# Kernel tuning notes

Hardware: AMD Instinct MI355X
Metric: run time of the kernel (lower is better)

The kernel has to match this reference:

```python
import jax, jax.numpy as jnp
import numpy as np
import math

D_MODEL = 1024
NHEAD = 16
D_HEAD = D_MODEL // NHEAD
TAU = 300.0
DELTA = 5.0 * 60.0  # delta_minutes -> seconds


def setup_inputs() -> dict:
    key = jax.random.key(0)
    ks = jax.random.split(key, 10)
    B, M = 4, 2048
    H = jax.random.normal(ks[0], (B, M, D_MODEL), dtype=jnp.float32)
    patch_mask = jax.random.randint(ks[1], (B, M), 0, 2).astype(jnp.int32)
    s = 1.0 / math.sqrt(D_MODEL)
    Wq = jax.random.normal(ks[2], (D_MODEL, D_MODEL), dtype=jnp.float32) * s
    bq = jnp.zeros((D_MODEL,), dtype=jnp.float32)
    Wk = jax.random.normal(ks[3], (D_MODEL, D_MODEL), dtype=jnp.float32) * s
    bk = jnp.zeros((D_MODEL,), dtype=jnp.float32)
    Wv = jax.random.normal(ks[4], (D_MODEL, D_MODEL), dtype=jnp.float32) * s
    bv = jnp.zeros((D_MODEL,), dtype=jnp.float32)
    Wo = jax.random.normal(ks[5], (D_MODEL, D_MODEL), dtype=jnp.float32) * s
    bo = jnp.zeros((D_MODEL,), dtype=jnp.float32)
    return {"H": H, "patch_mask": patch_mask, "Wq": Wq, "bq": bq,
            "Wk": Wk, "bk": bk, "Wv": Wv, "bv": bv, "Wo": Wo, "bo": bo}


def _time_bias(M):
    idx = jnp.arange(M)
    dist = jnp.abs(idx[:, None] - idx[None, :]).astype(jnp.float32) * DELTA
    w = jnp.exp(-dist / max(TAU, 1e-6))
    return jnp.log(w + 1e-12)  # (M, M)


def reference(H, patch_mask, Wq, bq, Wk, bk, Wv, bv, Wo, bo):
    B, M, D = H.shape
    nh, dh = NHEAD, D_HEAD
    # projections -> (B, nh, M, dh)
    q = (H @ Wq.T + bq).reshape(B, M, nh, dh).transpose(0, 2, 1, 3)
    k = (H @ Wk.T + bk).reshape(B, M, nh, dh).transpose(0, 2, 1, 3)
    v = (H @ Wv.T + bv).reshape(B, M, nh, dh).transpose(0, 2, 1, 3)
    attn = jnp.einsum('bhqd,bhkd->bhqk', q, k) / math.sqrt(dh)
    attn = attn + _time_bias(M)[None, None, :, :]
    key_pad = patch_mask <= 0  # (B, M)
    attn = jnp.where(key_pad[:, None, None, :], -1e9, attn)
    A = jax.nn.softmax(attn, axis=-1)
    out = jnp.einsum('bhqk,bhkd->bhqd', A, v)
    out = out.transpose(0, 2, 1, 3).reshape(B, M, D)
    out = out @ Wo.T + bo
    out = out * patch_mask[:, :, None].astype(out.dtype)
    return out
```

## Files before the change

kernel.cpp:

```cpp
#include <hip/hip_runtime.h>
#include <stdint.h>

typedef short short8 __attribute__((ext_vector_type(8)));
typedef float f32x4 __attribute__((ext_vector_type(4)));

#define B_    4
#define M_    2048
#define D_    1024
#define NH_   16
#define DH_   64
#define LOG2E 1.44269504f

__device__ __forceinline__ short f2bf(float f) {
  union { float f; uint32_t u; } v; v.f = f;
  uint32_t r = (v.u + 0x7fffu + ((v.u >> 16) & 1u)) >> 16;
  return (short)r;
}

__device__ __forceinline__ void gl_lds16(const void* g, void* l) {
  __builtin_amdgcn_global_load_lds(
      (__attribute__((address_space(1))) void*)(g),
      (__attribute__((address_space(3))) void*)(l),
      16, 0, 0);
}

__device__ __forceinline__ f32x4 mfma16(short8 a, short8 b, f32x4 c) {
  return __builtin_amdgcn_mfma_f32_16x16x32_bf16(a, b, c, 0, 0, 0);
}

__global__ __launch_bounds__(256) void cvt_all(const float* __restrict__ H,
                                               const float* __restrict__ s0,
                                               const float* __restrict__ s1,
                                               const float* __restrict__ s2,
                                               const float* __restrict__ s3,
                                               short* __restrict__ dH,
                                               short* __restrict__ d0,
                                               short* __restrict__ d1,
                                               short* __restrict__ d2,
                                               short* __restrict__ d3) {
  const int bidx = blockIdx.x;
  const float* src;
  short* dst;
  int i;
  if (bidx < 8192) {
    src = H; dst = dH; i = bidx * 256 + threadIdx.x;
  } else {
    const int y = (bidx - 8192) >> 10;
    src = (y == 0) ? s0 : (y == 1) ? s1 : (y == 2) ? s2 : s3;
    dst = (y == 0) ? d0 : (y == 1) ? d1 : (y == 2) ? d2 : d3;
    i = ((bidx - 8192) & 1023) * 256 + threadIdx.x;
  }
  float4 v = ((const float4*)src)[i];
  short4 o;
  o.x = f2bf(v.x); o.y = f2bf(v.y); o.z = f2bf(v.z); o.w = f2bf(v.w);
  ((short4*)dst)[i] = o;
}

__global__ __launch_bounds__(256, 2) void gemm_qkv(const short* __restrict__ A,
                                                   const short* __restrict__ Wqb,
                                                   const short* __restrict__ Wkb,
                                                   const short* __restrict__ Wvb,
                                                   const float* __restrict__ bq,
                                                   const float* __restrict__ bk,
                                                   const float* __restrict__ bv,
                                                   short* __restrict__ Qo,
                                                   short* __restrict__ Ko,
                                                   short* __restrict__ Vo) {
  __shared__ char smem_raw[65536];
  short* Ab0 = (short*)smem_raw;
  short* Ab1 = (short*)(smem_raw + 8192);

  const int L = blockIdx.x + 8 * blockIdx.y;
  const int xcd = L & 7;
  const int s = L >> 3;
  const int m_local = s & 7;
  const int nt = s >> 3;
  const int m0 = (xcd * 8 + m_local) * 128;
  const int n0 = nt * 128;

  const int tid = threadIdx.x;
  const int w = tid >> 6, l = tid & 63;
  const int q4 = l >> 4, c = l & 15;
  const int wr = w >> 1, wc = w & 1;

  f32x4 acc[3][4][4] = {};
  const int arow = (l >> 2);
  const int acol = ((l & 3) ^ ((l >> 3) & 3)) * 8;
  const int q4s = (q4 ^ ((c >> 1) & 3)) * 8;

  const short* Bz0 = Wqb;
  const short* Bz1 = Wkb;
  const short* Bz2 = Wvb;

#pragma unroll
  for (int st = 0; st < 2; ++st) {
    const int chunk = w * 2 + st;
    const size_t roff = (size_t)(chunk * 16 + arow) * 1024 + acol;
    gl_lds16(A + (size_t)m0 * 1024 + roff, Ab0 + chunk * 512);
    gl_lds16(Bz0 + (size_t)n0 * 1024 + roff, (short*)(smem_raw + 16384) + chunk * 512);
    gl_lds16(Bz1 + (size_t)n0 * 1024 + roff, (short*)(smem_raw + 32768) + chunk * 512);
    gl_lds16(Bz2 + (size_t)n0 * 1024 + roff, (short*)(smem_raw + 49152) + chunk * 512);
  }
  __syncthreads();

  for (int kk = 0; kk < 32; ++kk) {
    const int cur = kk & 1;
    if (kk + 1 < 32) {
      const int k0n = (kk + 1) * 32;
#pragma unroll
      for (int st = 0; st < 2; ++st) {
        const int chunk = w * 2 + st;
        const size_t roff = (size_t)(chunk * 16 + arow) * 1024 + k0n + acol;
        gl_lds16(A + (size_t)m0 * 1024 + roff, (cur ? Ab0 : Ab1) + chunk * 512);
        gl_lds16(Bz0 + (size_t)n0 * 1024 + roff,
                 (short*)(smem_raw + 16384 + (cur ? 0 : 8192)) + chunk * 512);
        gl_lds16(Bz1 + (size_t)n0 * 1024 + roff,
                 (short*)(smem_raw + 32768 + (cur ? 0 : 8192)) + chunk * 512);
        gl_lds16(Bz2 + (size_t)n0 * 1024 + roff,
                 (short*)(smem_raw + 49152 + (cur ? 0 : 8192)) + chunk * 512);
      }
    }
    const short* Ab = cur ? Ab1 : Ab0;
    short8 af[4];
#pragma unroll
    for (int i = 0; i < 4; ++i)
      af[i] = *(const short8*)(Ab + (wr * 64 + i * 16 + c) * 32 + q4s);
#pragma unroll
    for (int z = 0; z < 3; ++z) {
      const short* Bb =
          (const short*)(smem_raw + 16384 + z * 16384 + (cur ? 8192 : 0));
      short8 bfr[4];
#pragma unroll
      for (int j = 0; j < 4; ++j)
        bfr[j] = *(const short8*)(Bb + (wc * 64 + j * 16 + c) * 32 + q4s);
#pragma unroll
      for (int i = 0; i < 4; ++i)
#pragma unroll
        for (int j = 0; j < 4; ++j)
          acc[z][i][j] = mfma16(af[i], bfr[j], acc[z][i][j]);
    }
    __syncthreads();
  }

#pragma unroll
  for (int z = 0; z < 2; ++z) {
    short* Cb = (short*)smem_raw;
    const float* bias = z ? bk : bq;
    short* outp = z ? Ko : Qo;
    const float scale = z ? 1.0f : 0.125f;
#pragma unroll
    for (int j = 0; j < 4; ++j) {
      const float bvv = bias[n0 + wc * 64 + j * 16 + c];
#pragma unroll
      for (int i = 0; i < 4; ++i)
#pragma unroll
        for (int r = 0; r < 4; ++r)
          Cb[(wr * 64 + i * 16 + q4 * 4 + r) * 136 + wc * 64 + j * 16 + c] =
              f2bf((acc[z][i][j][r] + bvv) * scale);
    }
    __syncthreads();
#pragma unroll
    for (int p = 0; p < 8; ++p) {
      const int g = p * 256 + tid;
      const int row = g >> 4, seg = g & 15;
      *(short8*)(outp + (size_t)(m0 + row) * 1024 + n0 + seg * 8) =
          *(const short8*)(Cb + row * 136 + seg * 8);
    }
    __syncthreads();
  }
  {
    short* Cb = (short*)smem_raw;
#pragma unroll
    for (int j = 0; j < 4; ++j) {
      const float bvv = bv[n0 + wc * 64 + j * 16 + c];
#pragma unroll
      for (int i = 0; i < 4; ++i) {
        short4 pk;
        pk.x = f2bf(acc[2][i][j][0] + bvv);
        pk.y = f2bf(acc[2][i][j][1] + bvv);
        pk.z = f2bf(acc[2][i][j][2] + bvv);
        pk.w = f2bf(acc[2][i][j][3] + bvv);
        *(short4*)(Cb + (wc * 64 + j * 16 + c) * 136 + wr * 64 + i * 16 + q4 * 4) = pk;
      }
    }
    __syncthreads();
    const int bb = m0 >> 11;
    const int tokb = m0 & 2047;
#pragma unroll
    for (int p = 0; p < 8; ++p) {
      const int g = p * 256 + tid;
      const int col = g >> 4, rseg = g & 15;
      const int colg = n0 + col;
      const int hh = colg >> 6, dd = colg & 63;
      *(short8*)(Vo + ((size_t)(bb * NH_ + hh) * DH_ + dd) * M_ + tokb + rseg * 8) =
          *(const short8*)(Cb + col * 136 + rseg * 8);
    }
  }
}

__global__ __launch_bounds__(256, 2) void gemm_oproj(const short* __restrict__ A,
                                                     const short* __restrict__ Bt,
                                                     const float* __restrict__ bias,
                                                     const int* __restrict__ pmask,
                                                     float* __restrict__ outp) {
  __shared__ char smem[33792];
  short* Ab0 = (short*)smem;
  short* Ab1 = (short*)(smem + 8192);
  short* Bb0 = (short*)(smem + 16384);
  short* Bb1 = (short*)(smem + 24576);

  const int L = blockIdx.x + 8 * blockIdx.y;
  const int xcd = L & 7;
  const int s = L >> 3;
  const int m_local = s & 7;
  const int nt = s >> 3;
  const int m0 = (xcd * 8 + m_local) * 128;
  const int n0 = nt * 128;

  const int tid = threadIdx.x;
  const int w = tid >> 6, l = tid & 63;
  const int q4 = l >> 4, c = l & 15;
  const int wr = w >> 1, wc = w & 1;

  f32x4 acc[4][4] = {};
  const int arow = (l >> 2);
  const int acol = ((l & 3) ^ ((l >> 3) & 3)) * 8;
  const int q4s = (q4 ^ ((c >> 1) & 3)) * 8;

#pragma unroll
  for (int st = 0; st < 2; ++st) {
    const int chunk = w * 2 + st;
    const size_t roff = (size_t)(chunk * 16 + arow) * 1024 + acol;
    gl_lds16(A + (size_t)m0 * 1024 + roff, Ab0 + chunk * 512);
    gl_lds16(Bt + (size_t)n0 * 1024 + roff, Bb0 + chunk * 512);
  }
  __syncthreads();

  for (int kk = 0; kk < 32; ++kk) {
    const int cur = kk & 1;
    if (kk + 1 < 32) {
      const int k0n = (kk + 1) * 32;
#pragma unroll
      for (int st = 0; st < 2; ++st) {
        const int chunk = w * 2 + st;
        const size_t roff = (size_t)(chunk * 16 + arow) * 1024 + k0n + acol;
        gl_lds16(A + (size_t)m0 * 1024 + roff, (cur ? Ab0 : Ab1) + chunk * 512);
        gl_lds16(Bt + (size_t)n0 * 1024 + roff, (cur ? Bb0 : Bb1) + chunk * 512);
      }
    }
    const short* Ab = cur ? Ab1 : Ab0;
    const short* Bb = cur ? Bb1 : Bb0;
    short8 af[4], bfr[4];
#pragma unroll
    for (int i = 0; i < 4; ++i)
      af[i] = *(const short8*)(Ab + (wr * 64 + i * 16 + c) * 32 + q4s);
#pragma unroll
    for (int j = 0; j < 4; ++j)
      bfr[j] = *(const short8*)(Bb + (wc * 64 + j * 16 + c) * 32 + q4s);
#pragma unroll
    for (int i = 0; i < 4; ++i)
#pragma unroll
      for (int j = 0; j < 4; ++j)
        acc[i][j] = mfma16(af[i], bfr[j], acc[i][j]);
    __syncthreads();
  }

  float* Cf = (float*)smem;
#pragma unroll
  for (int half = 0; half < 2; ++half) {
    __syncthreads();
    if (wr == half) {
#pragma unroll
      for (int j = 0; j < 4; ++j) {
        const float bvv = bias[n0 + wc * 64 + j * 16 + c];
#pragma unroll
        for (int i = 0; i < 4; ++i)
#pragma unroll
          for (int r = 0; r < 4; ++r)
            Cf[(i * 16 + q4 * 4 + r) * 132 + wc * 64 + j * 16 + c] =
                acc[i][j][r] + bvv;
      }
    }
    __syncthreads();
#pragma unroll
    for (int p = 0; p < 8; ++p) {
      const int g = p * 256 + tid;
      const int row = g >> 5, seg = g & 31;
      const int rowg = m0 + half * 64 + row;
      const float mmv = (pmask[rowg] > 0) ? 1.0f : 0.0f;
      float4 v = *(const float4*)(Cf + row * 132 + seg * 4);
      v.x *= mmv; v.y *= mmv; v.z *= mmv; v.w *= mmv;
      *(float4*)(outp + (size_t)rowg * 1024 + n0 + seg * 4) = v;
    }
  }
}

__global__ __launch_bounds__(256) void attn_kernel(const short* __restrict__ Qb,
                                                   const short* __restrict__ Kb,
                                                   const short* __restrict__ Vtb,
                                                   const int* __restrict__ pmask,
                                                   short* __restrict__ Attb) {
  __shared__ char smem[20480];
  short* Ks0 = (short*)smem;
  short* Ks1 = (short*)(smem + 4096);
  short* Vs0 = (short*)(smem + 8192);
  short* Vs1 = (short*)(smem + 12288);
  short* Ps  = (short*)(smem + 16384);

  const int tid = threadIdx.x;
  const int w = tid >> 6, l = tid & 63;
  const int q4 = l >> 4, c = l & 15;
  const int qt = blockIdx.x, h = blockIdx.y, b = blockIdx.z;
  const short* Qrow = Qb + (size_t)(b * M_) * D_ + h * DH_;
  const short* Kbase = Kb + (size_t)(b * M_) * D_ + h * DH_;
  const short* Vbase = Vtb + (size_t)(b * NH_ + h) * DH_ * M_;
  const int qrow0 = qt * 64 + w * 16;

  short8 aq0 = *(const short8*)(Qrow + (size_t)(qrow0 + c) * D_ + q4 * 8);
  short8 aq1 = *(const short8*)(Qrow + (size_t)(qrow0 + c) * D_ + 32 + q4 * 8);

  const int jt0 = max(0, 2 * qt - 2);
  const int jt1 = min(M_ / 32 - 1, 2 * qt + 3);

  const int kh = tid >> 7, krow = (tid >> 2) & 31, ch = tid & 3;
  const int vrow = tid >> 2;

  {
    const int j0 = jt0 * 32;
    gl_lds16(Kbase + (size_t)(j0 + krow) * D_ + kh * 32 + ch * 8, (char*)Ks0 + tid * 16);
    gl_lds16(Vbase + (size_t)vrow * M_ + j0 + ch * 8, (char*)Vs0 + tid * 16);
  }
  __syncthreads();

  f32x4 o[4] = {};
  float lrun[4] = {0.f, 0.f, 0.f, 0.f};
  short* Pw = Ps + w * 512;

  for (int jt = jt0; jt <= jt1; ++jt) {
    const int buf = (jt - jt0) & 1;
    const int j0 = jt * 32;
    if (jt < jt1) {
      const int j0n = j0 + 32;
      gl_lds16(Kbase + (size_t)(j0n + krow) * D_ + kh * 32 + ch * 8,
               (char*)(buf ? Ks0 : Ks1) + tid * 16);
      gl_lds16(Vbase + (size_t)vrow * M_ + j0n + ch * 8,
               (char*)(buf ? Vs0 : Vs1) + tid * 16);
    }
    const short* Kt = buf ? Ks1 : Ks0;
    const short* Vt = buf ? Vs1 : Vs0;
    short8 b00 = *(const short8*)(Kt + c * 32 + q4 * 8);
    short8 b10 = *(const short8*)(Kt + 1024 + c * 32 + q4 * 8);
    short8 b01 = *(const short8*)(Kt + (16 + c) * 32 + q4 * 8);
    short8 b11 = *(const short8*)(Kt + 1024 + (16 + c) * 32 + q4 * 8);
    f32x4 s0 = {}, s1 = {};
    s0 = mfma16(aq0, b00, s0);
    s0 = mfma16(aq1, b10, s0);
    s1 = mfma16(aq0, b01, s1);
    s1 = mfma16(aq1, b11, s1);

    const float w0m = (pmask[b * M_ + j0 + c] > 0) ? 1.f : 0.f;
    const float w1m = (pmask[b * M_ + j0 + 16 + c] > 0) ? 1.f : 0.f;

#pragma unroll
    for (int r = 0; r < 4; ++r) {
      const int qr = qrow0 + q4 * 4 + r;
      const float d0 = fminf(fabsf((float)(qr - (j0 + c))), 28.0f);
      const float d1 = fminf(fabsf((float)(qr - (j0 + 16 + c))), 28.0f);
      const float p0 = exp2f((s0[r] - d0) * LOG2E) * w0m;
      const float p1 = exp2f((s1[r] - d1) * LOG2E) * w1m;
      Pw[(q4 * 4 + r) * 32 + c] = f2bf(p0);
      Pw[(q4 * 4 + r) * 32 + 16 + c] = f2bf(p1);
      lrun[r] += p0 + p1;
    }
    short8 pa = *(const short8*)(Pw + c * 32 + q4 * 8);
#pragma unroll
    for (int f = 0; f < 4; ++f) {
      short8 bv = *(const short8*)(Vt + (f * 16 + c) * 32 + q4 * 8);
      o[f] = mfma16(pa, bv, o[f]);
    }
    __syncthreads();
  }

#pragma unroll
  for (int r = 0; r < 4; ++r) {
#pragma unroll
    for (int off = 1; off < 16; off <<= 1)
      lrun[r] += __shfl_xor(lrun[r], off);
  }

  short* Cb = (short*)smem;
#pragma unroll
  for (int r = 0; r < 4; ++r) {
    const float inv = 1.0f / lrun[r];
#pragma unroll
    for (int f = 0; f < 4; ++f)
      Cb[(w * 16 + q4 * 4 + r) * 72 + f * 16 + c] = f2bf(o[f][r] * inv);
  }
  __syncthreads();
#pragma unroll
  for (int p = 0; p < 2; ++p) {
    const int u = p * 256 + tid;
    const int row = u >> 3, seg = u & 7;
    *(short8*)(Attb + (size_t)(b * M_ + qt * 64 + row) * D_ + h * DH_ + seg * 8) =
        *(const short8*)(Cb + row * 72 + seg * 8);
  }
}

extern "C" void kernel_launch(void* const* d_in, const int* in_sizes, int n_in,
                              void* d_out, int out_size, void* d_ws, size_t ws_size,
                              hipStream_t stream) {
  const float* H     = (const float*)d_in[0];
  const int*   pmask = (const int*)d_in[1];
  const float* Wq    = (const float*)d_in[2];
  const float* bq    = (const float*)d_in[3];
  const float* Wk    = (const float*)d_in[4];
  const float* bk    = (const float*)d_in[5];
  const float* Wv    = (const float*)d_in[6];
  const float* bv    = (const float*)d_in[7];
  const float* Wo    = (const float*)d_in[8];
  const float* bo    = (const float*)d_in[9];
  float* out = (float*)d_out;
  char* ws = (char*)d_ws;

  short* Hb   = (short*)(ws);
  short* Attb = (short*)(ws);
  short* Wqb  = (short*)(ws + (16u << 20));
  short* Wkb  = (short*)(ws + (18u << 20));
  short* Wvb  = (short*)(ws + (20u << 20));
  short* Wob  = (short*)(ws + (22u << 20));
  short* Qb   = (short*)(ws + (24u << 20));
  short* Kb2  = (short*)(ws + (40u << 20));
  short* Vtb  = (short*)(ws + (56u << 20));

  cvt_all<<<8192 + 4096, 256, 0, stream>>>(H, Wq, Wk, Wv, Wo,
                                           Hb, Wqb, Wkb, Wvb, Wob);

  gemm_qkv<<<dim3(8, 64), 256, 0, stream>>>(Hb, Wqb, Wkb, Wvb, bq, bk, bv,
                                            Qb, Kb2, Vtb);

  attn_kernel<<<dim3(M_ / 64, NH_, B_), 256, 0, stream>>>(Qb, Kb2, Vtb, pmask, Attb);

  gemm_oproj<<<dim3(8, 64), 256, 0, stream>>>(Attb, Wob, bo, pmask, out);
}
```

Measured before the change: 209.6 us.

## Fold log2e into Q scale, use raw exp2, and hand-pipeline K/V loads with vmcnt

Folds the LOG2E factor into the Q projection scale and the distance bias, so the softmax exponent becomes a single native exp2 with no multiply. Replaces the __syncthreads at the top and bottom of the attention loop with explicit s_waitcnt vmcnt plus s_barrier, so the global-to-LDS prefetch of the next K/V tile can stay in flight while the current tile is computed. Also raises wave priority around the MFMA sections. The manual vmcnt counting relies on exactly two outstanding loads per iteration, and any other in-flight global load (the pmask reads, or the initial Q loads) could make the count wrong and introduce a race.

```diff
diff --git a/kernel.cpp b/kernel.cpp
--- a/kernel.cpp
+++ b/kernel.cpp
@@ -11,6 +11,12 @@
 #define DH_   64
 #define LOG2E 1.44269504f
 
+#if __has_builtin(__builtin_amdgcn_exp2f)
+#define EXP2F(x) __builtin_amdgcn_exp2f(x)
+#else
+#define EXP2F(x) exp2f(x)
+#endif
+
 __device__ __forceinline__ short f2bf(float f) {
   union { float f; uint32_t u; } v; v.f = f;
   uint32_t r = (v.u + 0x7fffu + ((v.u >> 16) & 1u)) >> 16;
@@ -27,6 +33,8 @@
 __device__ __forceinline__ f32x4 mfma16(short8 a, short8 b, f32x4 c) {
   return __builtin_amdgcn_mfma_f32_16x16x32_bf16(a, b, c, 0, 0, 0);
 }
+
+#define VM_WAIT(N)  asm volatile("s_waitcnt vmcnt(" #N ")" ::: "memory")
 
 __global__ __launch_bounds__(256) void cvt_all(const float* __restrict__ H,
                                                const float* __restrict__ s0,
@@ -147,7 +155,7 @@
     short* Cb = (short*)smem_raw;
     const float* bias = z ? bk : bq;
     short* outp = z ? Ko : Qo;
-    const float scale = z ? 1.0f : 0.125f;
+    const float scale = z ? 1.0f : (0.125f * LOG2E);
 #pragma unroll
     for (int j = 0; j < 4; ++j) {
       const float bvv = bias[n0 + wc * 64 + j * 16 + c];
@@ -314,6 +322,7 @@
   const short* Qrow = Qb + (size_t)(b * M_) * D_ + h * DH_;
   const short* Kbase = Kb + (size_t)(b * M_) * D_ + h * DH_;
   const short* Vbase = Vtb + (size_t)(b * NH_ + h) * DH_ * M_;
+  const int* pm = pmask + b * M_;
   const int qrow0 = qt * 64 + w * 16;
 
   short8 aq0 = *(const short8*)(Qrow + (size_t)(qrow0 + c) * D_ + q4 * 8);
@@ -330,11 +339,13 @@
     gl_lds16(Kbase + (size_t)(j0 + krow) * D_ + kh * 32 + ch * 8, (char*)Ks0 + tid * 16);
     gl_lds16(Vbase + (size_t)vrow * M_ + j0 + ch * 8, (char*)Vs0 + tid * 16);
   }
-  __syncthreads();
 
   f32x4 o[4] = {};
   float lrun[4] = {0.f, 0.f, 0.f, 0.f};
   short* Pw = Ps + w * 512;
+  const int ib = qrow0 + q4 * 4 - c;
+  const float CLAMP = 28.0f * LOG2E;
+  const float C16   = 16.0f * LOG2E;
 
   for (int jt = jt0; jt <= jt1; ++jt) {
     const int buf = (jt - jt0) & 1;
@@ -345,7 +356,14 @@
                (char*)(buf ? Ks0 : Ks1) + tid * 16);
       gl_lds16(Vbase + (size_t)vrow * M_ + j0n + ch * 8,
                (char*)(buf ? Vs0 : Vs1) + tid * 16);
-    }
+      VM_WAIT(2);
+    } else {
+      VM_WAIT(0);
+    }
+    __builtin_amdgcn_sched_barrier(0);
+    __builtin_amdgcn_s_barrier();
+    __builtin_amdgcn_sched_barrier(0);
+
     const short* Kt = buf ? Ks1 : Ks0;
     const short* Vt = buf ? Vs1 : Vs0;
     short8 b00 = *(const short8*)(Kt + c * 32 + q4 * 8);
@@ -353,32 +371,38 @@
     short8 b01 = *(const short8*)(Kt + (16 + c) * 32 + q4 * 8);
     short8 b11 = *(const short8*)(Kt + 1024 + (16 + c) * 32 + q4 * 8);
     f32x4 s0 = {}, s1 = {};
+    __builtin_amdgcn_s_setprio(1);
     s0 = mfma16(aq0, b00, s0);
     s0 = mfma16(aq1, b10, s0);
     s1 = mfma16(aq0, b01, s1);
     s1 = mfma16(aq1, b11, s1);
-
-    const float w0m = (pmask[b * M_ + j0 + c] > 0) ? 1.f : 0.f;
-    const float w1m = (pmask[b * M_ + j0 + 16 + c] > 0) ? 1.f : 0.f;
+    __builtin_amdgcn_s_setprio(0);
+
+    const float w0m = (pm[j0 + c] > 0) ? 1.f : 0.f;
+    const float w1m = (pm[j0 + 16 + c] > 0) ? 1.f : 0.f;
+    const float eb = (float)(ib - j0) * LOG2E;
 
 #pragma unroll
     for (int r = 0; r < 4; ++r) {
-      const int qr = qrow0 + q4 * 4 + r;
-      const float d0 = fminf(fabsf((float)(qr - (j0 + c))), 28.0f);
-      const float d1 = fminf(fabsf((float)(qr - (j0 + 16 + c))), 28.0f);
-      const float p0 = exp2f((s0[r] - d0) * LOG2E) * w0m;
-      const float p1 = exp2f((s1[r] - d1) * LOG2E) * w1m;
+      const float er = eb + (float)r * LOG2E;
+      const float d0 = fminf(fabsf(er), CLAMP);
+      const float d1 = fminf(fabsf(er - C16), CLAMP);
+      const float p0 = EXP2F(s0[r] - d0) * w0m;
+      const float p1 = EXP2F(s1[r] - d1) * w1m;
       Pw[(q4 * 4 + r) * 32 + c] = f2bf(p0);
       Pw[(q4 * 4 + r) * 32 + 16 + c] = f2bf(p1);
       lrun[r] += p0 + p1;
     }
     short8 pa = *(const short8*)(Pw + c * 32 + q4 * 8);
+    __builtin_amdgcn_s_setprio(1);
 #pragma unroll
     for (int f = 0; f < 4; ++f) {
       short8 bv = *(const short8*)(Vt + (f * 16 + c) * 32 + q4 * 8);
       o[f] = mfma16(pa, bv, o[f]);
     }
-    __syncthreads();
+    __builtin_amdgcn_s_setprio(0);
+    __builtin_amdgcn_sched_barrier(0);
+    __builtin_amdgcn_s_barrier();
   }
 
 #pragma unroll
```

Result: no change. 208.6 us, median of 2 (-0.5%).
